# Kernel tuning notes

Measured on AMD Instinct MI355X. Metric: run time of the kernel, lower is better.

The kernel has to match this reference:

```python
import jax, jax.numpy as jnp
import numpy as np

B, T, HID = 2, 2048, 2048
NH = 8
D = HID // NH  # head_dim = 256 (expand_ratio=1 so input_dim == hidden_size)
EPS_RMS = 1e-8   # RMSNorm inside BitLinear
EPS_LN = 1e-5    # layernorm_eps for g_norm


def _rms(x, w, eps):
    # weighted RMSNorm over last dim
    return x * jax.lax.rsqrt(jnp.mean(x * x, axis=-1, keepdims=True) + eps) * w


def _act_quant(x):
    # per-token 8-bit fake quant with straight-through estimator
    s = 127.0 / jnp.clip(jnp.max(jnp.abs(x), axis=-1, keepdims=True), 1e-5)
    q = jnp.clip(jnp.round(x * s), -128, 127) / s
    return x + jax.lax.stop_gradient(q - x)


def _weight_quant(w):
    # ternary weight quantization (BitNet b1.58) with STE
    s = 1.0 / jnp.clip(jnp.mean(jnp.abs(w)), 1e-5)
    q = jnp.clip(jnp.round(w * s), -1, 1) / s
    return w + jax.lax.stop_gradient(q - w)


def _bitlinear(x, w, norm_w):
    # FusedBitLinear: RMSNorm -> activation quant -> ternary-weight linear
    xq = _act_quant(_rms(x, norm_w, EPS_RMS))
    return jnp.einsum('btk,ok->bto', xq, _weight_quant(w))


def setup_inputs() -> dict:
    key = jax.random.key(0)
    ks = jax.random.split(key, 5)
    std = 2 ** (-2.5) * np.sqrt(2.0 / (HID + HID))  # xavier_uniform-ish std with gain 2^-2.5
    return {
        'hidden_states': jax.random.normal(ks[0], (B, T, HID), dtype=jnp.float32),
        'w_i': jax.random.normal(ks[1], (HID, HID), dtype=jnp.float32) * std,
        'w_f': jax.random.normal(ks[2], (HID, HID), dtype=jnp.float32) * std,
        'w_g': jax.random.normal(ks[3], (HID, HID), dtype=jnp.float32) * std,
        'w_o': jax.random.normal(ks[4], (HID, HID), dtype=jnp.float32) * std,
        'n_i': jnp.ones((HID,), jnp.float32),
        'n_f': jnp.ones((HID,), jnp.float32),
        'n_g': jnp.ones((HID,), jnp.float32),
        'n_o': jnp.ones((HID,), jnp.float32),
        'gn_w': jnp.ones((HID,), jnp.float32),
    }


def reference(hidden_states, w_i, w_f, w_g, w_o, n_i, n_f, n_g, n_o, gn_w):
    hs = hidden_states
    i = _bitlinear(hs, w_i, n_i)                      # [B,T,HID]
    f = jax.nn.sigmoid(_bitlinear(hs, w_f, n_f))      # forget gate
    # swiglu(i, 1 - f) = silu(i) * (1 - f)
    i = i * jax.nn.sigmoid(i) * (1.0 - f)

    # b l (h d) -> t b h d for scan
    def to_tbhd(x):
        return x.reshape(B, T, NH, D).transpose(1, 0, 2, 3)

    i_t, f_t = to_tbhd(i), to_tbhd(f)

    def step(h, ft_it):
        ft, it = ft_it
        h = ft * h + it
        return h, h

    h0 = jnp.zeros((B, NH, D), dtype=i.dtype)
    _, o = jax.lax.scan(step, h0, (f_t, i_t))         # [T,B,NH,D]
    o = o.transpose(1, 0, 2, 3).reshape(B, T, HID)     # b l (h d)

    # g_norm(g_proj(hs), o): rmsnorm(g) * o * sigmoid(o)
    g = _bitlinear(hs, w_g, n_g)
    o = _rms(g, gn_w, EPS_LN) * o * jax.nn.sigmoid(o)
    return _bitlinear(o, w_o, n_o)
```

## Files before the change

### kernel.cpp

```cpp
#include <hip/hip_runtime.h>
#include <math.h>

#define HID 2048
#define TOKENS 4096
#define TT 2048
#define NCH 4096
#define NC 32
#define CL 64
#define WELEM 4194304

typedef unsigned short u16;
typedef signed char i8;
typedef int i32x4 __attribute__((ext_vector_type(4)));

__device__ inline float sigm(float x) { return 1.0f / (1.0f + expf(-x)); }

__device__ inline float wred_sum(float v) {
#pragma unroll
  for (int o = 32; o > 0; o >>= 1) v += __shfl_down(v, o);
  return v;
}
__device__ inline float wred_max(float v) {
#pragma unroll
  for (int o = 32; o > 0; o >>= 1) v = fmaxf(v, __shfl_down(v, o));
  return v;
}
__device__ inline double wred_sumd(double v) {
#pragma unroll
  for (int o = 32; o > 0; o >>= 1) v += __shfl_down(v, o);
  return v;
}

__device__ __forceinline__ void gl_lds16(const void* g, void* l) {
  __builtin_amdgcn_global_load_lds(
      (__attribute__((address_space(1))) void*)(void*)g,
      (__attribute__((address_space(3))) void*)l, 16, 0, 0);
}

__device__ __forceinline__ int pack8(const int* qi) {
  return (qi[0] & 255) | ((qi[1] & 255) << 8) | ((qi[2] & 255) << 16)
       | ((qi[3] & 255) << 24);
}

__global__ __launch_bounds__(256) void absmean_kernel(
    const float* __restrict__ w0, const float* __restrict__ w1,
    const float* __restrict__ w2, const float* __restrict__ w3,
    double* __restrict__ wsum) {
  int widx = blockIdx.x >> 9;
  int blk = blockIdx.x & 511;
  const float* w = widx == 0 ? w0 : widx == 1 ? w1 : widx == 2 ? w2 : w3;
  size_t base = (size_t)blk * 8192;
  double acc = 0.0;
#pragma unroll
  for (int r = 0; r < 8; ++r) {
    float4 v = *(const float4*)&w[base + (size_t)(r * 256 + threadIdx.x) * 4];
    acc += (double)fabsf(v.x) + (double)fabsf(v.y) + (double)fabsf(v.z) +
           (double)fabsf(v.w);
  }
  acc = wred_sumd(acc);
  __shared__ double sh[4];
  int tid = threadIdx.x;
  if ((tid & 63) == 0) sh[tid >> 6] = acc;
  __syncthreads();
  if (tid == 0) atomicAdd(&wsum[widx], (sh[0] + sh[1]) + (sh[2] + sh[3]));
}

__global__ __launch_bounds__(256) void wquant2_kernel(
    const float* __restrict__ wA, const float* __restrict__ wB,
    const double* __restrict__ wsum, int widxA, int widxB,
    i8* __restrict__ wqA, i8* __restrict__ wqB) {
  int sel = blockIdx.x >> 11;
  int blk = blockIdx.x & 2047;
  const float* w = sel ? wB : wA;
  i8* wq = sel ? wqB : wqA;
  int widx = sel ? widxB : widxA;
  double mean = wsum[widx] * (1.0 / (double)WELEM);
  float s = (float)(1.0 / fmax(mean, 1e-5));
  size_t base = (size_t)blk * 2048 + (size_t)threadIdx.x * 8;
  float4 va = *(const float4*)&w[base];
  float4 vb = *(const float4*)&w[base + 4];
  float vv[8] = {va.x, va.y, va.z, va.w, vb.x, vb.y, vb.z, vb.w};
  int qi[8];
#pragma unroll
  for (int j = 0; j < 8; ++j) {
    float q1 = rintf(vv[j] * s);
    q1 = fminf(fmaxf(q1, -1.0f), 1.0f);
    qi[j] = (int)q1;
  }
  *(int2*)&wq[base] = make_int2(pack8(qi), pack8(qi + 4));
}

__global__ __launch_bounds__(256) void rmsquant_kernel(
    const float* __restrict__ X, const float* __restrict__ nw,
    i8* __restrict__ Xq, float* __restrict__ inv_s) {
  int tok = blockIdx.x;
  int tid = threadIdx.x;
  const float* xrow = X + (size_t)tok * HID;
  int c0 = tid * 8;
  float x[8];
  *(float4*)&x[0] = *(const float4*)&xrow[c0];
  *(float4*)&x[4] = *(const float4*)&xrow[c0 + 4];
  float ss = 0.0f;
#pragma unroll
  for (int j = 0; j < 8; ++j) ss += x[j] * x[j];
  __shared__ float sh[4];
  float v = wred_sum(ss);
  if ((tid & 63) == 0) sh[tid >> 6] = v;
  __syncthreads();
  float tot = (sh[0] + sh[1]) + (sh[2] + sh[3]);
  float rstd = (float)(1.0 / sqrt((double)(tot * (1.0f / HID)) + 1e-8));
  float y[8];
  float amax = 0.0f;
#pragma unroll
  for (int j = 0; j < 8; ++j) {
    y[j] = x[j] * rstd * nw[c0 + j];
    amax = fmaxf(amax, fabsf(y[j]));
  }
  __syncthreads();
  v = wred_max(amax);
  if ((tid & 63) == 0) sh[tid >> 6] = v;
  __syncthreads();
  float am = fmaxf(fmaxf(fmaxf(sh[0], sh[1]), fmaxf(sh[2], sh[3])), 1e-5f);
  float s = 127.0f / am;
  int qi[8];
#pragma unroll
  for (int j = 0; j < 8; ++j) {
    float qq = rintf(y[j] * s);
    qq = fminf(fmaxf(qq, -128.0f), 127.0f);
    qi[j] = (int)qq;
  }
  *(int2*)&Xq[(size_t)tok * HID + c0] = make_int2(pack8(qi), pack8(qi + 4));
  if (tid == 0) inv_s[tok] = am * (1.0f / 127.0f);
}

__global__ __launch_bounds__(256) void rmsquant2_kernel(
    const float* __restrict__ X, const float* __restrict__ nw0,
    const float* __restrict__ nw1, i8* __restrict__ Xq0, i8* __restrict__ Xq1,
    float* __restrict__ inv0, float* __restrict__ inv1) {
  int tok = blockIdx.x;
  int tid = threadIdx.x;
  const float* xrow = X + (size_t)tok * HID;
  int c0 = tid * 8;
  float x[8];
  *(float4*)&x[0] = *(const float4*)&xrow[c0];
  *(float4*)&x[4] = *(const float4*)&xrow[c0 + 4];
  float ss = 0.0f;
#pragma unroll
  for (int j = 0; j < 8; ++j) ss += x[j] * x[j];
  __shared__ float sh[4];
  float v = wred_sum(ss);
  if ((tid & 63) == 0) sh[tid >> 6] = v;
  __syncthreads();
  float tot = (sh[0] + sh[1]) + (sh[2] + sh[3]);
  float rstd = (float)(1.0 / sqrt((double)(tot * (1.0f / HID)) + 1e-8));
#pragma unroll
  for (int pass = 0; pass < 2; ++pass) {
    const float* nw = pass == 0 ? nw0 : nw1;
    i8* Xq = pass == 0 ? Xq0 : Xq1;
    float* inv_s = pass == 0 ? inv0 : inv1;
    float y[8];
    float amax = 0.0f;
#pragma unroll
    for (int j = 0; j < 8; ++j) {
      y[j] = x[j] * rstd * nw[c0 + j];
      amax = fmaxf(amax, fabsf(y[j]));
    }
    __syncthreads();
    float vv = wred_max(amax);
    if ((tid & 63) == 0) sh[tid >> 6] = vv;
    __syncthreads();
    float am = fmaxf(fmaxf(fmaxf(sh[0], sh[1]), fmaxf(sh[2], sh[3])), 1e-5f);
    float s = 127.0f / am;
    int qi[8];
#pragma unroll
    for (int j = 0; j < 8; ++j) {
      float qq = rintf(y[j] * s);
      qq = fminf(fmaxf(qq, -128.0f), 127.0f);
      qi[j] = (int)qq;
    }
    *(int2*)&Xq[(size_t)tok * HID + c0] = make_int2(pack8(qi), pack8(qi + 4));
    if (tid == 0) inv_s[tok] = am * (1.0f / 127.0f);
  }
}

__global__ __launch_bounds__(512) void gemm8_kernel(
    const i8* __restrict__ A0, const i8* __restrict__ A1,
    const i8* __restrict__ W0, const i8* __restrict__ W1,
    const float* __restrict__ inv0, const float* __restrict__ inv1,
    const double* __restrict__ wsum, int widx0, int widx1,
    float* __restrict__ O0, float* __restrict__ O1, int mode0, int mode1) {
  const int tid = threadIdx.x;
  const int cpx = gridDim.x >> 3;
  const int lid = blockIdx.x;
  const int swz = (lid & 7) * cpx + (lid >> 3);
  const int seg = swz >> 9;
  const int idx = swz & 511;
  const int n0 = (idx & 15) * 128;
  const int m0 = (idx >> 4) * 128;

  const i8* Aq = seg ? A1 : A0;
  const i8* Wq = seg ? W1 : W0;
  const float* inv_s = seg ? inv1 : inv0;
  float* Out = seg ? O1 : O0;
  const int mode = seg ? mode1 : mode0;
  const int widx = seg ? widx1 : widx0;

  __shared__ __align__(16) i8 As[2][8192];
  __shared__ __align__(16) i8 Bs[2][8192];
  float wscale = (float)fmax(wsum[widx] * (1.0 / (double)WELEM), 1e-5);

  const int wave = tid >> 6, lane = tid & 63;
  const int wm = wave >> 2;
  const int wn = wave & 3;
  const int lrow = lane & 15;
  const int ksel = lane >> 4;
  const int gr = (lrow >> 1) & 3;
  const int srl = lane >> 2;
  const int sg = (lane >> 3) & 3;
  const int skoff = ((lane & 3) ^ sg) << 4;

  const i8* Ab = Aq + (size_t)m0 * HID;
  const i8* Wb = Wq + (size_t)n0 * HID;

  i32x4 acc[4][2];
#pragma unroll
  for (int i = 0; i < 4; ++i)
#pragma unroll
    for (int j = 0; j < 2; ++j)
#pragma unroll
      for (int r = 0; r < 4; ++r) acc[i][j][r] = 0;

#define STAGE(buf, k0)                                                       \
  {                                                                          \
    int row = wave * 16 + srl;                                               \
    gl_lds16(&Ab[(size_t)row * HID + (k0) + skoff], &As[buf][wave * 1024]);  \
    gl_lds16(&Wb[(size_t)row * HID + (k0) + skoff], &Bs[buf][wave * 1024]);  \
  }

  const int NT = HID / 64;
  STAGE(0, 0)
  __syncthreads();
  int cur = 0;
  for (int kt = 0; kt < NT; ++kt) {
    if (kt + 1 < NT) STAGE(cur ^ 1, (kt + 1) * 64)
    i32x4 af[4], bfr[2];
#pragma unroll
    for (int i = 0; i < 4; ++i) {
      int ra = wm * 64 + i * 16 + lrow;
      af[i] = *(const i32x4*)&As[cur][ra * 64 + ((ksel ^ gr) << 4)];
    }
#pragma unroll
    for (int j = 0; j < 2; ++j) {
      int rb = wn * 32 + j * 16 + lrow;
      bfr[j] = *(const i32x4*)&Bs[cur][rb * 64 + ((ksel ^ gr) << 4)];
    }
    __builtin_amdgcn_s_setprio(1);
#pragma unroll
    for (int i = 0; i < 4; ++i)
#pragma unroll
      for (int j = 0; j < 2; ++j)
        acc[i][j] = __builtin_amdgcn_mfma_i32_16x16x64_i8(af[i], bfr[j],
                                                          acc[i][j], 0, 0, 0);
    __builtin_amdgcn_s_setprio(0);
    __syncthreads();
    cur ^= 1;
  }
#undef STAGE

#pragma unroll
  for (int i = 0; i < 4; ++i) {
    int rbase = m0 + wm * 64 + i * 16 + (lane >> 4) * 4;
#pragma unroll
    for (int j = 0; j < 2; ++j) {
      int col = n0 + wn * 32 + j * 16 + lrow;
#pragma unroll
      for (int r = 0; r < 4; ++r) {
        int row = rbase + r;
        float v = (float)acc[i][j][r] * inv_s[row] * wscale;
        size_t oidx = (size_t)row * HID + col;
        if (mode == 0) {
          Out[oidx] = sigm(v);
        } else if (mode == 1) {
          Out[oidx] = v * sigm(v);
        } else {
          Out[oidx] = v;
        }
      }
    }
  }
}

__global__ __launch_bounds__(256) void scan1_kernel(
    const float* __restrict__ F, float* __restrict__ IO, float* __restrict__ P,
    float* __restrict__ H) {
  int c = blockIdx.x * 256 + threadIdx.x;
  int q = blockIdx.y;
  size_t base =
      (size_t)(c >> 11) * TT * HID + (c & 2047) + (size_t)q * CL * HID;
  float h = 0.0f, p = 1.0f;
#pragma unroll 4
  for (int t = 0; t < CL; ++t) {
    size_t idx = base + (size_t)t * HID;
    float f = F[idx];
    float iv = IO[idx];
    h = fmaf(f, h, iv - iv * f);
    p *= f;
    IO[idx] = h;
  }
  P[q * NCH + c] = p;
  H[q * NCH + c] = h;
}

__global__ __launch_bounds__(256) void scan2_kernel(
    const float* __restrict__ P, const float* __restrict__ H,
    float* __restrict__ Ini) {
  int c = blockIdx.x * 256 + threadIdx.x;
  float carry = 0.0f;
#pragma unroll
  for (int q = 0; q < NC; ++q) {
    float pq = P[q * NCH + c];
    float hq = H[q * NCH + c];
    Ini[q * NCH + c] = carry;
    carry = fmaf(pq, carry, hq);
  }
}

__global__ __launch_bounds__(256) void scan3_kernel(
    const float* __restrict__ F, const float* __restrict__ Ini,
    float* __restrict__ IO) {
  int c = blockIdx.x * 256 + threadIdx.x;
  int q = blockIdx.y + 1;
  float h0 = Ini[q * NCH + c];
  if (h0 == 0.0f) return;
  size_t base =
      (size_t)(c >> 11) * TT * HID + (c & 2047) + (size_t)q * CL * HID;
  float p = 1.0f;
#pragma unroll 4
  for (int t = 0; t < CL; ++t) {
    size_t idx = base + (size_t)t * HID;
    p *= F[idx];
    IO[idx] = fmaf(p, h0, IO[idx]);
  }
}

__global__ __launch_bounds__(256) void combine_quant_kernel(
    const float* __restrict__ G, const float* __restrict__ gnw,
    const float* __restrict__ O, const float* __restrict__ nw,
    i8* __restrict__ Xq, float* __restrict__ inv_s) {
  int tok = blockIdx.x;
  int tid = threadIdx.x;
  int c0 = tid * 8;
  const float* grow = G + (size_t)tok * HID;
  const float* orow = O + (size_t)tok * HID;
  float g[8], o[8];
  *(float4*)&g[0] = *(const float4*)&grow[c0];
  *(float4*)&g[4] = *(const float4*)&grow[c0 + 4];
  *(float4*)&o[0] = *(const float4*)&orow[c0];
  *(float4*)&o[4] = *(const float4*)&orow[c0 + 4];
  __shared__ float sh[4];
  float ss = 0.0f;
#pragma unroll
  for (int j = 0; j < 8; ++j) ss += g[j] * g[j];
  float v = wred_sum(ss);
  if ((tid & 63) == 0) sh[tid >> 6] = v;
  __syncthreads();
  float tot = (sh[0] + sh[1]) + (sh[2] + sh[3]);
  float rstd_g = (float)(1.0 / sqrt((double)(tot * (1.0f / HID)) + 1e-5));
  float on[8];
  float ss2 = 0.0f;
#pragma unroll
  for (int j = 0; j < 8; ++j) {
    on[j] = g[j] * rstd_g * gnw[c0 + j] * o[j] * sigm(o[j]);
    ss2 += on[j] * on[j];
  }
  __syncthreads();
  v = wred_sum(ss2);
  if ((tid & 63) == 0) sh[tid >> 6] = v;
  __syncthreads();
  float tot2 = (sh[0] + sh[1]) + (sh[2] + sh[3]);
  float rstd_o = (float)(1.0 / sqrt((double)(tot2 * (1.0f / HID)) + 1e-8));
  float y[8];
  float amax = 0.0f;
#pragma unroll
  for (int j = 0; j < 8; ++j) {
    y[j] = on[j] * rstd_o * nw[c0 + j];
    amax = fmaxf(amax, fabsf(y[j]));
  }
  __syncthreads();
  v = wred_max(amax);
  if ((tid & 63) == 0) sh[tid >> 6] = v;
  __syncthreads();
  float am = fmaxf(fmaxf(fmaxf(sh[0], sh[1]), fmaxf(sh[2], sh[3])), 1e-5f);
  float s = 127.0f / am;
  int qi[8];
#pragma unroll
  for (int j = 0; j < 8; ++j) {
    float qq = rintf(y[j] * s);
    qq = fminf(fmaxf(qq, -128.0f), 127.0f);
    qi[j] = (int)qq;
  }
  *(int2*)&Xq[(size_t)tok * HID + c0] = make_int2(pack8(qi), pack8(qi + 4));
  if (tid == 0) inv_s[tok] = am * (1.0f / 127.0f);
}

extern "C" void kernel_launch(void* const* d_in, const int* in_sizes, int n_in,
                              void* d_out, int out_size, void* d_ws,
                              size_t ws_size, hipStream_t stream) {
  const float* hs = (const float*)d_in[0];
  const float* w_i = (const float*)d_in[1];
  const float* w_f = (const float*)d_in[2];
  const float* w_g = (const float*)d_in[3];
  const float* w_o = (const float*)d_in[4];
  const float* n_i = (const float*)d_in[5];
  const float* n_f = (const float*)d_in[6];
  const float* n_g = (const float*)d_in[7];
  const float* n_o = (const float*)d_in[8];
  const float* gn_w = (const float*)d_in[9];
  float* Out = (float*)d_out;

  char* ws = (char*)d_ws;
  i8* WQ0 = (i8*)ws;
  i8* WQ1 = (i8*)(ws + 4194304);
  i8* XQ0 = (i8*)(ws + 8388608);
  i8* XQ1 = (i8*)(ws + 16777216);
  float* F = (float*)(ws + 25165824);
  float* G = F;
  float* invs0 = (float*)(ws + 58720256);
  float* invs1 = (float*)(ws + 58736640);
  double* wsum = (double*)(ws + 58753024);
  float* scanP = (float*)(ws + 58754048);
  float* scanH = (float*)(ws + 59278336);

  hipMemsetAsync(wsum, 0, 4 * sizeof(double), stream);
  absmean_kernel<<<2048, 256, 0, stream>>>(w_i, w_f, w_g, w_o, wsum);

  wquant2_kernel<<<4096, 256, 0, stream>>>(w_f, w_i, wsum, 1, 0, WQ0, WQ1);
  rmsquant2_kernel<<<TOKENS, 256, 0, stream>>>(hs, n_f, n_i, XQ0, XQ1, invs0,
                                               invs1);

  gemm8_kernel<<<1024, 512, 0, stream>>>(XQ0, XQ1, WQ0, WQ1, invs0, invs1,
                                         wsum, 1, 0, F, Out, 0, 1);

  wquant2_kernel<<<4096, 256, 0, stream>>>(w_g, w_o, wsum, 2, 3, WQ0, WQ1);
  rmsquant_kernel<<<TOKENS, 256, 0, stream>>>(hs, n_g, XQ0, invs0);

  scan1_kernel<<<dim3(NCH / 256, NC), 256, 0, stream>>>(F, Out, scanP, scanH);
  scan2_kernel<<<NCH / 256, 256, 0, stream>>>(scanP, scanH, scanP);
  scan3_kernel<<<dim3(NCH / 256, NC - 1), 256, 0, stream>>>(F, scanP, Out);

  gemm8_kernel<<<512, 512, 0, stream>>>(XQ0, XQ0, WQ0, WQ0, invs0, invs0, wsum,
                                        2, 2, G, G, 2, 2);

  combine_quant_kernel<<<TOKENS, 256, 0, stream>>>(G, gn_w, Out, n_o, XQ1,
                                                   invs1);

  gemm8_kernel<<<512, 512, 0, stream>>>(XQ1, XQ1, WQ1, WQ1, invs1, invs1, wsum,
                                        3, 3, Out, Out, 2, 2);
}
```

Measured before the change: 245.4 us.

## Enlarge int8 GEMM tile to 128x256 with 4 waves and 128x64 per-wave tiles

The int8 MFMA GEMM moves from a 128x128 tile with 8 waves (64x32 each) to a 128x256 tile with 4 waves, each computing 128x64. Every wave reuses all 8 A fragments across 4 B fragments, which raises MFMA work per LDS read and halves the number of blocks. The staging loop is rewritten so each wave issues up to 6 global-to-LDS chunk loads. In exchange, accumulator register pressure grows (32 i32x4 accumulators per lane), LDS use rises to 48KB per block, and the grid shrinks, which can cut occupancy and the ability to hide latency.

```diff
diff --git a/kernel.cpp b/kernel.cpp
--- a/kernel.cpp
+++ b/kernel.cpp
@@ -183,7 +183,7 @@
   }
 }
 
-__global__ __launch_bounds__(512) void gemm8_kernel(
+__global__ __launch_bounds__(256, 2) void gemm4_kernel(
     const i8* __restrict__ A0, const i8* __restrict__ A1,
     const i8* __restrict__ W0, const i8* __restrict__ W1,
     const float* __restrict__ inv0, const float* __restrict__ inv1,
@@ -193,10 +193,10 @@
   const int cpx = gridDim.x >> 3;
   const int lid = blockIdx.x;
   const int swz = (lid & 7) * cpx + (lid >> 3);
-  const int seg = swz >> 9;
-  const int idx = swz & 511;
-  const int n0 = (idx & 15) * 128;
-  const int m0 = (idx >> 4) * 128;
+  const int seg = swz >> 8;
+  const int idx = swz & 255;
+  const int n0 = (idx & 7) * 256;
+  const int m0 = (idx >> 3) * 128;
 
   const i8* Aq = seg ? A1 : A0;
   const i8* Wq = seg ? W1 : W0;
@@ -206,12 +206,10 @@
   const int widx = seg ? widx1 : widx0;
 
   __shared__ __align__(16) i8 As[2][8192];
-  __shared__ __align__(16) i8 Bs[2][8192];
+  __shared__ __align__(16) i8 Bs[2][16384];
   float wscale = (float)fmax(wsum[widx] * (1.0 / (double)WELEM), 1e-5);
 
   const int wave = tid >> 6, lane = tid & 63;
-  const int wm = wave >> 2;
-  const int wn = wave & 3;
   const int lrow = lane & 15;
   const int ksel = lane >> 4;
   const int gr = (lrow >> 1) & 3;
@@ -222,19 +220,28 @@
   const i8* Ab = Aq + (size_t)m0 * HID;
   const i8* Wb = Wq + (size_t)n0 * HID;
 
-  i32x4 acc[4][2];
-#pragma unroll
-  for (int i = 0; i < 4; ++i)
-#pragma unroll
-    for (int j = 0; j < 2; ++j)
+  i32x4 acc[8][4];
+#pragma unroll
+  for (int i = 0; i < 8; ++i)
+#pragma unroll
+    for (int j = 0; j < 4; ++j)
 #pragma unroll
       for (int r = 0; r < 4; ++r) acc[i][j][r] = 0;
 
-#define STAGE(buf, k0)                                                       \
-  {                                                                          \
-    int row = wave * 16 + srl;                                               \
-    gl_lds16(&Ab[(size_t)row * HID + (k0) + skoff], &As[buf][wave * 1024]);  \
-    gl_lds16(&Wb[(size_t)row * HID + (k0) + skoff], &Bs[buf][wave * 1024]);  \
+#define STAGE(buf, k0)                                                        \
+  {                                                                           \
+    _Pragma("unroll") for (int c = 0; c < 6; ++c) {                           \
+      int chunk = wave * 6 + c;                                               \
+      if (chunk < 8) {                                                        \
+        int row = chunk * 16 + srl;                                           \
+        gl_lds16(&Ab[(size_t)row * HID + (k0) + skoff],                       \
+                 &As[buf][chunk * 1024]);                                     \
+      } else {                                                                \
+        int row = (chunk - 8) * 16 + srl;                                     \
+        gl_lds16(&Wb[(size_t)row * HID + (k0) + skoff],                       \
+                 &Bs[buf][(chunk - 8) * 1024]);                               \
+      }                                                                       \
+    }                                                                         \
   }
 
   const int NT = HID / 64;
@@ -243,22 +250,22 @@
   int cur = 0;
   for (int kt = 0; kt < NT; ++kt) {
     if (kt + 1 < NT) STAGE(cur ^ 1, (kt + 1) * 64)
-    i32x4 af[4], bfr[2];
-#pragma unroll
-    for (int i = 0; i < 4; ++i) {
-      int ra = wm * 64 + i * 16 + lrow;
+    i32x4 af[8], bfr[4];
+#pragma unroll
+    for (int i = 0; i < 8; ++i) {
+      int ra = i * 16 + lrow;
       af[i] = *(const i32x4*)&As[cur][ra * 64 + ((ksel ^ gr) << 4)];
     }
 #pragma unroll
-    for (int j = 0; j < 2; ++j) {
-      int rb = wn * 32 + j * 16 + lrow;
+    for (int j = 0; j < 4; ++j) {
+      int rb = wave * 64 + j * 16 + lrow;
       bfr[j] = *(const i32x4*)&Bs[cur][rb * 64 + ((ksel ^ gr) << 4)];
     }
     __builtin_amdgcn_s_setprio(1);
 #pragma unroll
-    for (int i = 0; i < 4; ++i)
-#pragma unroll
-      for (int j = 0; j < 2; ++j)
+    for (int i = 0; i < 8; ++i)
+#pragma unroll
+      for (int j = 0; j < 4; ++j)
         acc[i][j] = __builtin_amdgcn_mfma_i32_16x16x64_i8(af[i], bfr[j],
                                                           acc[i][j], 0, 0, 0);
     __builtin_amdgcn_s_setprio(0);
@@ -268,11 +275,11 @@
 #undef STAGE
 
 #pragma unroll
-  for (int i = 0; i < 4; ++i) {
-    int rbase = m0 + wm * 64 + i * 16 + (lane >> 4) * 4;
-#pragma unroll
-    for (int j = 0; j < 2; ++j) {
-      int col = n0 + wn * 32 + j * 16 + lrow;
+  for (int i = 0; i < 8; ++i) {
+    int rbase = m0 + i * 16 + (lane >> 4) * 4;
+#pragma unroll
+    for (int j = 0; j < 4; ++j) {
+      int col = n0 + wave * 64 + j * 16 + lrow;
 #pragma unroll
       for (int r = 0; r < 4; ++r) {
         int row = rbase + r;
@@ -438,8 +445,8 @@
   rmsquant2_kernel<<<TOKENS, 256, 0, stream>>>(hs, n_f, n_i, XQ0, XQ1, invs0,
                                                invs1);
 
-  gemm8_kernel<<<1024, 512, 0, stream>>>(XQ0, XQ1, WQ0, WQ1, invs0, invs1,
-                                         wsum, 1, 0, F, Out, 0, 1);
+  gemm4_kernel<<<512, 256, 0, stream>>>(XQ0, XQ1, WQ0, WQ1, invs0, invs1, wsum,
+                                        1, 0, F, Out, 0, 1);
 
   wquant2_kernel<<<4096, 256, 0, stream>>>(w_g, w_o, wsum, 2, 3, WQ0, WQ1);
   rmsquant_kernel<<<TOKENS, 256, 0, stream>>>(hs, n_g, XQ0, invs0);
@@ -448,12 +455,12 @@
   scan2_kernel<<<NCH / 256, 256, 0, stream>>>(scanP, scanH, scanP);
   scan3_kernel<<<dim3(NCH / 256, NC - 1), 256, 0, stream>>>(F, scanP, Out);
 
-  gemm8_kernel<<<512, 512, 0, stream>>>(XQ0, XQ0, WQ0, WQ0, invs0, invs0, wsum,
+  gemm4_kernel<<<256, 256, 0, stream>>>(XQ0, XQ0, WQ0, WQ0, invs0, invs0, wsum,
                                         2, 2, G, G, 2, 2);
 
   combine_quant_kernel<<<TOKENS, 256, 0, stream>>>(G, gn_w, Out, n_o, XQ1,
                                                    invs1);
 
-  gemm8_kernel<<<512, 512, 0, stream>>>(XQ1, XQ1, WQ1, WQ1, invs1, invs1, wsum,
+  gemm4_kernel<<<256, 256, 0, stream>>>(XQ1, XQ1, WQ1, WQ1, invs1, invs1, wsum,
                                         3, 3, Out, Out, 2, 2);
 }
```

Result: slower. 272.2 us (+10.9%).

## Replace LDS-staged int8 GEMM with direct register-loaded double-buffered fragments

Applied to the files above, without the earlier changes.

The int8 MFMA GEMM no longer stages tiles through LDS with global_load_lds and per-iteration barriers. Each wave now loads its A and B fragments directly from global memory into registers, using two register sets for software pipelining. Waves drop from 8 to 4 per block, and each wave computes a 64x64 sub-tile instead of 64x32. This removes the LDS traffic and block synchronisation. The cost is duplicated global/L2 reads across waves, since no data is shared through LDS, plus higher register pressure.

```diff
diff --git a/kernel.cpp b/kernel.cpp
--- a/kernel.cpp
+++ b/kernel.cpp
@@ -29,12 +29,6 @@
 #pragma unroll
   for (int o = 32; o > 0; o >>= 1) v += __shfl_down(v, o);
   return v;
-}
-
-__device__ __forceinline__ void gl_lds16(const void* g, void* l) {
-  __builtin_amdgcn_global_load_lds(
-      (__attribute__((address_space(1))) void*)(void*)g,
-      (__attribute__((address_space(3))) void*)l, 16, 0, 0);
 }
 
 __device__ __forceinline__ int pack8(const int* qi) {
@@ -183,7 +177,7 @@
   }
 }
 
-__global__ __launch_bounds__(512) void gemm8_kernel(
+__global__ __launch_bounds__(256, 3) void gemmr_kernel(
     const i8* __restrict__ A0, const i8* __restrict__ A1,
     const i8* __restrict__ W0, const i8* __restrict__ W1,
     const float* __restrict__ inv0, const float* __restrict__ inv1,
@@ -205,74 +199,66 @@
   const int mode = seg ? mode1 : mode0;
   const int widx = seg ? widx1 : widx0;
 
-  __shared__ __align__(16) i8 As[2][8192];
-  __shared__ __align__(16) i8 Bs[2][8192];
   float wscale = (float)fmax(wsum[widx] * (1.0 / (double)WELEM), 1e-5);
 
   const int wave = tid >> 6, lane = tid & 63;
-  const int wm = wave >> 2;
-  const int wn = wave & 3;
+  const int wm = wave >> 1, wn = wave & 1;
   const int lrow = lane & 15;
-  const int ksel = lane >> 4;
-  const int gr = (lrow >> 1) & 3;
-  const int srl = lane >> 2;
-  const int sg = (lane >> 3) & 3;
-  const int skoff = ((lane & 3) ^ sg) << 4;
-
-  const i8* Ab = Aq + (size_t)m0 * HID;
-  const i8* Wb = Wq + (size_t)n0 * HID;
-
-  i32x4 acc[4][2];
+  const int lk = (lane >> 4) * 16;
+
+  const i8* pA = Aq + (size_t)(m0 + wm * 64 + lrow) * HID + lk;
+  const i8* pB = Wq + (size_t)(n0 + wn * 64 + lrow) * HID + lk;
+
+  i32x4 acc[4][4];
 #pragma unroll
   for (int i = 0; i < 4; ++i)
 #pragma unroll
-    for (int j = 0; j < 2; ++j)
+    for (int j = 0; j < 4; ++j)
 #pragma unroll
       for (int r = 0; r < 4; ++r) acc[i][j][r] = 0;
 
-#define STAGE(buf, k0)                                                       \
-  {                                                                          \
-    int row = wave * 16 + srl;                                               \
-    gl_lds16(&Ab[(size_t)row * HID + (k0) + skoff], &As[buf][wave * 1024]);  \
-    gl_lds16(&Wb[(size_t)row * HID + (k0) + skoff], &Bs[buf][wave * 1024]);  \
+  i32x4 aA0, aA1, aA2, aA3, aB0, aB1, aB2, aB3;
+  i32x4 bA0, bA1, bA2, bA3, bB0, bB1, bB2, bB3;
+
+#define LOADS(P, K0)                                   \
+  P##A0 = *(const i32x4*)(pA + 0 * 16 * HID + (K0));   \
+  P##A1 = *(const i32x4*)(pA + 1 * 16 * HID + (K0));   \
+  P##A2 = *(const i32x4*)(pA + 2 * 16 * HID + (K0));   \
+  P##A3 = *(const i32x4*)(pA + 3 * 16 * HID + (K0));   \
+  P##B0 = *(const i32x4*)(pB + 0 * 16 * HID + (K0));   \
+  P##B1 = *(const i32x4*)(pB + 1 * 16 * HID + (K0));   \
+  P##B2 = *(const i32x4*)(pB + 2 * 16 * HID + (K0));   \
+  P##B3 = *(const i32x4*)(pB + 3 * 16 * HID + (K0));
+
+#define MFMAS(P)                                                       \
+  {                                                                    \
+    i32x4 _af[4] = {P##A0, P##A1, P##A2, P##A3};                       \
+    i32x4 _bf[4] = {P##B0, P##B1, P##B2, P##B3};                       \
+    __builtin_amdgcn_s_setprio(1);                                     \
+    _Pragma("unroll") for (int i = 0; i < 4; ++i)                      \
+        _Pragma("unroll") for (int j = 0; j < 4; ++j) acc[i][j] =      \
+            __builtin_amdgcn_mfma_i32_16x16x64_i8(_af[i], _bf[j],      \
+                                                  acc[i][j], 0, 0, 0); \
+    __builtin_amdgcn_s_setprio(0);                                     \
   }
 
   const int NT = HID / 64;
-  STAGE(0, 0)
-  __syncthreads();
-  int cur = 0;
-  for (int kt = 0; kt < NT; ++kt) {
-    if (kt + 1 < NT) STAGE(cur ^ 1, (kt + 1) * 64)
-    i32x4 af[4], bfr[2];
-#pragma unroll
-    for (int i = 0; i < 4; ++i) {
-      int ra = wm * 64 + i * 16 + lrow;
-      af[i] = *(const i32x4*)&As[cur][ra * 64 + ((ksel ^ gr) << 4)];
-    }
-#pragma unroll
-    for (int j = 0; j < 2; ++j) {
-      int rb = wn * 32 + j * 16 + lrow;
-      bfr[j] = *(const i32x4*)&Bs[cur][rb * 64 + ((ksel ^ gr) << 4)];
-    }
-    __builtin_amdgcn_s_setprio(1);
-#pragma unroll
-    for (int i = 0; i < 4; ++i)
-#pragma unroll
-      for (int j = 0; j < 2; ++j)
-        acc[i][j] = __builtin_amdgcn_mfma_i32_16x16x64_i8(af[i], bfr[j],
-                                                          acc[i][j], 0, 0, 0);
-    __builtin_amdgcn_s_setprio(0);
-    __syncthreads();
-    cur ^= 1;
-  }
-#undef STAGE
+  LOADS(a, 0)
+  for (int kt = 0; kt < NT; kt += 2) {
+    LOADS(b, (kt + 1) * 64)
+    MFMAS(a)
+    if (kt + 2 < NT) LOADS(a, (kt + 2) * 64)
+    MFMAS(b)
+  }
+#undef LOADS
+#undef MFMAS
 
 #pragma unroll
   for (int i = 0; i < 4; ++i) {
     int rbase = m0 + wm * 64 + i * 16 + (lane >> 4) * 4;
 #pragma unroll
-    for (int j = 0; j < 2; ++j) {
-      int col = n0 + wn * 32 + j * 16 + lrow;
+    for (int j = 0; j < 4; ++j) {
+      int col = n0 + wn * 64 + j * 16 + lrow;
 #pragma unroll
       for (int r = 0; r < 4; ++r) {
         int row = rbase + r;
@@ -438,7 +424,7 @@
   rmsquant2_kernel<<<TOKENS, 256, 0, stream>>>(hs, n_f, n_i, XQ0, XQ1, invs0,
                                                invs1);
 
-  gemm8_kernel<<<1024, 512, 0, stream>>>(XQ0, XQ1, WQ0, WQ1, invs0, invs1,
+  gemmr_kernel<<<1024, 256, 0, stream>>>(XQ0, XQ1, WQ0, WQ1, invs0, invs1,
                                          wsum, 1, 0, F, Out, 0, 1);
 
   wquant2_kernel<<<4096, 256, 0, stream>>>(w_g, w_o, wsum, 2, 3, WQ0, WQ1);
@@ -448,12 +434,12 @@
   scan2_kernel<<<NCH / 256, 256, 0, stream>>>(scanP, scanH, scanP);
   scan3_kernel<<<dim3(NCH / 256, NC - 1), 256, 0, stream>>>(F, scanP, Out);
 
-  gemm8_kernel<<<512, 512, 0, stream>>>(XQ0, XQ0, WQ0, WQ0, invs0, invs0, wsum,
+  gemmr_kernel<<<512, 256, 0, stream>>>(XQ0, XQ0, WQ0, WQ0, invs0, invs0, wsum,
                                         2, 2, G, G, 2, 2);
 
   combine_quant_kernel<<<TOKENS, 256, 0, stream>>>(G, gn_w, Out, n_o, XQ1,
                                                    invs1);
 
-  gemm8_kernel<<<512, 512, 0, stream>>>(XQ1, XQ1, WQ1, WQ1, invs1, invs1, wsum,
+  gemmr_kernel<<<512, 256, 0, stream>>>(XQ1, XQ1, WQ1, WQ1, invs1, invs1, wsum,
                                         3, 3, Out, Out, 2, 2);
 }
```

New measurement: 393.6 us. 60.4% more time.

## Double K-tile depth to 128 in int8 GEMM and split fused dual launch

Applied to the files above, without the earlier changes.

The int8 MFMA GEMM now stages 128-wide K tiles instead of 64. That halves the number of barrier-separated iterations and doubles the MFMAs per sync, using a new 8-way XOR swizzle for the wider LDS rows. The fused two-segment launch for the i/f projections is split into two separate 512-block launches, and the segment selection logic is removed. LDS use doubles to 64 KB per block, which may reduce occupancy, and the split launch gives up the concurrency the combined grid had.

```diff
diff --git a/kernel.cpp b/kernel.cpp
--- a/kernel.cpp
+++ b/kernel.cpp
@@ -184,29 +184,17 @@
 }
 
 __global__ __launch_bounds__(512) void gemm8_kernel(
-    const i8* __restrict__ A0, const i8* __restrict__ A1,
-    const i8* __restrict__ W0, const i8* __restrict__ W1,
-    const float* __restrict__ inv0, const float* __restrict__ inv1,
-    const double* __restrict__ wsum, int widx0, int widx1,
-    float* __restrict__ O0, float* __restrict__ O1, int mode0, int mode1) {
+    const i8* __restrict__ Aq, const i8* __restrict__ Wq,
+    const float* __restrict__ inv_s, const double* __restrict__ wsum, int widx,
+    float* __restrict__ Out, int mode) {
   const int tid = threadIdx.x;
-  const int cpx = gridDim.x >> 3;
   const int lid = blockIdx.x;
-  const int swz = (lid & 7) * cpx + (lid >> 3);
-  const int seg = swz >> 9;
-  const int idx = swz & 511;
-  const int n0 = (idx & 15) * 128;
-  const int m0 = (idx >> 4) * 128;
-
-  const i8* Aq = seg ? A1 : A0;
-  const i8* Wq = seg ? W1 : W0;
-  const float* inv_s = seg ? inv1 : inv0;
-  float* Out = seg ? O1 : O0;
-  const int mode = seg ? mode1 : mode0;
-  const int widx = seg ? widx1 : widx0;
-
-  __shared__ __align__(16) i8 As[2][8192];
-  __shared__ __align__(16) i8 Bs[2][8192];
+  const int swz = (lid & 7) * 64 + (lid >> 3);
+  const int n0 = (swz & 15) * 128;
+  const int m0 = (swz >> 4) * 128;
+
+  __shared__ __align__(16) i8 As[2][16384];
+  __shared__ __align__(16) i8 Bs[2][16384];
   float wscale = (float)fmax(wsum[widx] * (1.0 / (double)WELEM), 1e-5);
 
   const int wave = tid >> 6, lane = tid & 63;
@@ -214,10 +202,9 @@
   const int wn = wave & 3;
   const int lrow = lane & 15;
   const int ksel = lane >> 4;
-  const int gr = (lrow >> 1) & 3;
-  const int srl = lane >> 2;
-  const int sg = (lane >> 3) & 3;
-  const int skoff = ((lane & 3) ^ sg) << 4;
+  const int rsw = lrow & 7;
+  const int srow8 = lane >> 3;
+  const int scol = ((lane & 7) ^ srow8) << 4;
 
   const i8* Ab = Aq + (size_t)m0 * HID;
   const i8* Wb = Wq + (size_t)n0 * HID;
@@ -230,37 +217,50 @@
 #pragma unroll
       for (int r = 0; r < 4; ++r) acc[i][j][r] = 0;
 
-#define STAGE(buf, k0)                                                       \
-  {                                                                          \
-    int row = wave * 16 + srl;                                               \
-    gl_lds16(&Ab[(size_t)row * HID + (k0) + skoff], &As[buf][wave * 1024]);  \
-    gl_lds16(&Wb[(size_t)row * HID + (k0) + skoff], &Bs[buf][wave * 1024]);  \
-  }
-
-  const int NT = HID / 64;
+#define STAGE(buf, k0)                                                      \
+  {                                                                         \
+    _Pragma("unroll") for (int c = 0; c < 2; ++c) {                         \
+      int chunk = wave * 2 + c;                                             \
+      int row = chunk * 8 + srow8;                                          \
+      gl_lds16(&Ab[(size_t)row * HID + (k0) + scol], &As[buf][chunk * 1024]); \
+      gl_lds16(&Wb[(size_t)row * HID + (k0) + scol], &Bs[buf][chunk * 1024]); \
+    }                                                                       \
+  }
+
+  const int NT = HID / 128;
   STAGE(0, 0)
   __syncthreads();
   int cur = 0;
   for (int kt = 0; kt < NT; ++kt) {
-    if (kt + 1 < NT) STAGE(cur ^ 1, (kt + 1) * 64)
-    i32x4 af[4], bfr[2];
+    if (kt + 1 < NT) STAGE(cur ^ 1, (kt + 1) * 128)
+    i32x4 af[4][2], bfr[2][2];
 #pragma unroll
     for (int i = 0; i < 4; ++i) {
       int ra = wm * 64 + i * 16 + lrow;
-      af[i] = *(const i32x4*)&As[cur][ra * 64 + ((ksel ^ gr) << 4)];
+#pragma unroll
+      for (int kk = 0; kk < 2; ++kk) {
+        int phys = ((kk << 2) | ksel) ^ rsw;
+        af[i][kk] = *(const i32x4*)&As[cur][ra * 128 + phys * 16];
+      }
     }
 #pragma unroll
     for (int j = 0; j < 2; ++j) {
       int rb = wn * 32 + j * 16 + lrow;
-      bfr[j] = *(const i32x4*)&Bs[cur][rb * 64 + ((ksel ^ gr) << 4)];
+#pragma unroll
+      for (int kk = 0; kk < 2; ++kk) {
+        int phys = ((kk << 2) | ksel) ^ rsw;
+        bfr[j][kk] = *(const i32x4*)&Bs[cur][rb * 128 + phys * 16];
+      }
     }
     __builtin_amdgcn_s_setprio(1);
 #pragma unroll
-    for (int i = 0; i < 4; ++i)
-#pragma unroll
-      for (int j = 0; j < 2; ++j)
-        acc[i][j] = __builtin_amdgcn_mfma_i32_16x16x64_i8(af[i], bfr[j],
-                                                          acc[i][j], 0, 0, 0);
+    for (int kk = 0; kk < 2; ++kk)
+#pragma unroll
+      for (int i = 0; i < 4; ++i)
+#pragma unroll
+        for (int j = 0; j < 2; ++j)
+          acc[i][j] = __builtin_amdgcn_mfma_i32_16x16x64_i8(
+              af[i][kk], bfr[j][kk], acc[i][j], 0, 0, 0);
     __builtin_amdgcn_s_setprio(0);
     __syncthreads();
     cur ^= 1;
@@ -438,8 +438,8 @@
   rmsquant2_kernel<<<TOKENS, 256, 0, stream>>>(hs, n_f, n_i, XQ0, XQ1, invs0,
                                                invs1);
 
-  gemm8_kernel<<<1024, 512, 0, stream>>>(XQ0, XQ1, WQ0, WQ1, invs0, invs1,
-                                         wsum, 1, 0, F, Out, 0, 1);
+  gemm8_kernel<<<512, 512, 0, stream>>>(XQ0, WQ0, invs0, wsum, 1, F, 0);
+  gemm8_kernel<<<512, 512, 0, stream>>>(XQ1, WQ1, invs1, wsum, 0, Out, 1);
 
   wquant2_kernel<<<4096, 256, 0, stream>>>(w_g, w_o, wsum, 2, 3, WQ0, WQ1);
   rmsquant_kernel<<<TOKENS, 256, 0, stream>>>(hs, n_g, XQ0, invs0);
@@ -448,12 +448,10 @@
   scan2_kernel<<<NCH / 256, 256, 0, stream>>>(scanP, scanH, scanP);
   scan3_kernel<<<dim3(NCH / 256, NC - 1), 256, 0, stream>>>(F, scanP, Out);
 
-  gemm8_kernel<<<512, 512, 0, stream>>>(XQ0, XQ0, WQ0, WQ0, invs0, invs0, wsum,
-                                        2, 2, G, G, 2, 2);
+  gemm8_kernel<<<512, 512, 0, stream>>>(XQ0, WQ0, invs0, wsum, 2, G, 2);
 
   combine_quant_kernel<<<TOKENS, 256, 0, stream>>>(G, gn_w, Out, n_o, XQ1,
                                                    invs1);
 
-  gemm8_kernel<<<512, 512, 0, stream>>>(XQ1, XQ1, WQ1, WQ1, invs1, invs1, wsum,
-                                        3, 3, Out, Out, 2, 2);
-}
+  gemm8_kernel<<<512, 512, 0, stream>>>(XQ1, WQ1, invs1, wsum, 3, Out, 2);
+}
```

After: 236.8 us. 1.04x faster.
